# Optimization experiments

Hardware: AMD Instinct MI355X
Metric: run time of the kernel (lower is better)

The kernel has to match this reference:

```python
import math
import jax, jax.numpy as jnp
import numpy as np

N, E, H, D, NNZ = 32768, 512, 8, 64, 524288


def setup_inputs() -> dict:
    key = jax.random.key(0)
    ks = jax.random.split(key, 12)
    x = jax.random.normal(ks[0], (N, E), dtype=jnp.float32)
    row_index = jnp.sort(jax.random.randint(ks[1], (NNZ,), 0, N))
    col_index = jax.random.randint(ks[2], (NNZ,), 0, N)
    to_col_index = jax.random.randint(ks[3], (N,), 0, N)
    att_bias = jax.random.normal(ks[4], (H, NNZ), dtype=jnp.float32)
    # positive interatomic distances in ~[0.5, 5.5)
    dist = jax.random.uniform(ks[5], (NNZ,), dtype=jnp.float32) * 5.0 + 0.5
    pos = jax.random.normal(ks[6], (N, 3), dtype=jnp.float32)
    col_pos = jax.random.normal(ks[7], (N, 3), dtype=jnp.float32)
    s = 1.0 / math.sqrt(E)
    q_w = jax.random.normal(ks[8], (E, E), dtype=jnp.float32) * s
    q_b = jax.random.normal(ks[9], (E,), dtype=jnp.float32) * 0.02
    k_w = jax.random.normal(ks[10], (E, E), dtype=jnp.float32) * s
    k_b = jax.random.normal(ks[11], (E,), dtype=jnp.float32) * 0.02
    return {"x": x, "row_index": row_index, "col_index": col_index,
            "to_col_index": to_col_index, "att_bias": att_bias, "dist": dist,
            "pos": pos, "col_pos": col_pos,
            "q_w": q_w, "q_b": q_b, "k_w": k_w, "k_b": k_b}


def reference(x, row_index, col_index, to_col_index, att_bias, dist, pos, col_pos,
              q_w, q_b, k_w, k_b):
    n = x.shape[0]
    h = att_bias.shape[0]
    d = x.shape[1] // h
    # per-head projections: [N, H, D]
    q = (x @ q_w.T + q_b).reshape(n, h, d) * (1.0 / math.sqrt(d))
    k = (x @ k_w.T + k_b).reshape(n, h, d)[to_col_index]  # [Nk, H, D]
    # sparse (COO) masked q @ k^T plus additive bias -> per-edge logits [nnz, H]
    logits = jnp.einsum('ehd,ehd->eh', q[row_index], k[col_index]) + att_bias.T
    # sparse softmax over each query row (per head)
    m = jax.ops.segment_max(logits, row_index, num_segments=n)       # [N, H]
    p = jnp.exp(logits - m[row_index])
    z = jax.ops.segment_sum(p, row_index, num_segments=n)            # [N, H]
    att = p / z[row_index]                                           # [nnz, H]
    # distance-weighted attention (dist==0 -> contribution 0, as x/inf in torch)
    inv_d = jnp.where(dist == 0, 0.0, 1.0 / dist)
    att = att * inv_d[:, None]
    # sparse bmm against col_pos values and against ones
    cp = col_pos[col_index]                                          # [nnz, 3]
    dst_vec = jax.ops.segment_sum(att[:, :, None] * cp[:, None, :],
                                  row_index, num_segments=n)         # [N, H, 3]
    avg_inv_dist = jax.ops.segment_sum(att, row_index, num_segments=n)  # [N, H]
    src_vec = avg_inv_dist[..., None] * pos[:, None, :]              # [N, H, 3]
    v = dst_vec - src_vec
    norm = jnp.sqrt(jnp.sum(v * v, axis=-1, keepdims=True))
    feat3 = v / jnp.maximum(norm, 1e-12)                             # F.normalize
    feat = jnp.concatenate([feat3, avg_inv_dist[..., None]], axis=-1)  # [N, H, 4]
    return feat.reshape(n, h * 4)
```

## Files before the change

kernel.cpp:

```cpp
#include <hip/hip_runtime.h>
#include <math.h>
#include <stdint.h>

#define N_NODES 32768
#define E_DIM   512
#define H_HEADS 8
#define D_HEAD  64
#define NNZ_E   524288

typedef __attribute__((ext_vector_type(4))) float f32x4;
typedef __attribute__((ext_vector_type(8))) _Float16 f16x8;
typedef __attribute__((ext_vector_type(8))) short s16x8;

__device__ __forceinline__ void async16(const void* g, void* l) {
  __builtin_amdgcn_global_load_lds(
      (const __attribute__((address_space(1))) void*)g,
      (__attribute__((address_space(3))) void*)l, 16, 0, 0);
}

__global__ __launch_bounds__(256) void prep_small(
    const float* __restrict__ x,
    const float* __restrict__ q_w, const float* __restrict__ k_w,
    const int* __restrict__ row_index, const int* __restrict__ col_index,
    const int* __restrict__ to_col,
    _Float16* __restrict__ wq_h, _Float16* __restrict__ wk_h,
    _Float16* __restrict__ xs,
    int* __restrict__ row_start, int* __restrict__ ge) {
  const int b = blockIdx.x;
  if (b < 8448) {
    const float* src;
    _Float16* dst;
    int t;
    if (b < 128)      { src = q_w; dst = wq_h; t = b * 256 + threadIdx.x; }
    else if (b < 256) { src = k_w; dst = wk_h; t = (b - 128) * 256 + threadIdx.x; }
    else              { src = x;   dst = xs;   t = (b - 256) * 256 + threadIdx.x; }
    const int r = t >> 6;
    const int c8 = (t & 63) << 3;
    const float4 v0 = *(const float4*)(src + (size_t)r * 512 + c8);
    const float4 v1 = *(const float4*)(src + (size_t)r * 512 + c8 + 4);
    f16x8 o;
    o[0] = (_Float16)v0.x; o[1] = (_Float16)v0.y;
    o[2] = (_Float16)v0.z; o[3] = (_Float16)v0.w;
    o[4] = (_Float16)v1.x; o[5] = (_Float16)v1.y;
    o[6] = (_Float16)v1.z; o[7] = (_Float16)v1.w;
    *(f16x8*)(dst + (size_t)r * 512 + c8) = o;
  } else {
    const int e = (b - 8448) * 256 + threadIdx.x;
    if (e < NNZ_E) {
      ge[e] = to_col[col_index[e]];
      const int r0 = row_index[e];
      const int r1 = (e + 1 < NNZ_E) ? row_index[e + 1] : N_NODES;
      if (e == 0)
        for (int r = 0; r <= r0; ++r) row_start[r] = 0;
      for (int r = r0 + 1; r <= r1; ++r) row_start[r] = e + 1;
    }
  }
}

__global__ __launch_bounds__(256) void gemm_mfma(
    const _Float16* __restrict__ xs,
    const _Float16* __restrict__ wqh,
    const _Float16* __restrict__ wkh,
    const float* __restrict__ q_b, const float* __restrict__ k_b,
    short* __restrict__ q16, short* __restrict__ k16) {
  __shared__ _Float16 Ah[128 * 32];
  __shared__ _Float16 Bh[128 * 32];
  const int tid = threadIdx.x;
  const int w = tid >> 6;
  const int l = tid & 63;

  const int b = blockIdx.x;
  const int j = b >> 3;
  const int mb = (b & 7) * 32 + (j >> 3);
  const int c = j & 7;
  const bool is_q = ((c & 1) == 0);
  const int bm = mb * 128;
  const int bn = (c >> 1) * 128;

  const _Float16* __restrict__ wmat = is_q ? wqh : wkh;
  const float* __restrict__ bias = is_q ? q_b : k_b;
  short* __restrict__ outp = is_q ? q16 : k16;
  const float oscale = is_q ? 2048.f : 4096.f;

  const int wm = (w & 1) * 64;
  const int wn = (w >> 1) * 64;

  f32x4 acc[4][4];
#pragma unroll
  for (int i = 0; i < 4; ++i)
#pragma unroll
    for (int jj = 0; jj < 4; ++jj) acc[i][jj] = (f32x4){0.f, 0.f, 0.f, 0.f};

  const int sr0 = w * 16 + (l >> 2);
  const int sr1 = sr0 + 64;
  const int sc = (((l & 3) ^ ((l >> 3) & 3)) << 3);
  const int fr = l & 15;
  const int fcs = ((((l >> 4) ^ ((fr >> 1) & 3)) & 3) << 3);

  const _Float16* __restrict__ wa = wmat + (size_t)bn * 512;
  const _Float16* __restrict__ xa = xs + (size_t)bm * 512;

  for (int k0 = 0; k0 < 512; k0 += 32) {
    async16(xa + (size_t)sr0 * 512 + k0 + sc, Ah + w * 512);
    async16(xa + (size_t)sr1 * 512 + k0 + sc, Ah + (w + 4) * 512);
    async16(wa + (size_t)sr0 * 512 + k0 + sc, Bh + w * 512);
    async16(wa + (size_t)sr1 * 512 + k0 + sc, Bh + (w + 4) * 512);
    __syncthreads();

    f16x8 av[4], bv[4];
#pragma unroll
    for (int i = 0; i < 4; ++i)
      av[i] = *(const f16x8*)(Ah + (wm + i * 16 + fr) * 32 + fcs);
#pragma unroll
    for (int i = 0; i < 4; ++i)
      bv[i] = *(const f16x8*)(Bh + (wn + i * 16 + fr) * 32 + fcs);
#pragma unroll
    for (int i = 0; i < 4; ++i)
#pragma unroll
      for (int jj = 0; jj < 4; ++jj)
        acc[i][jj] = __builtin_amdgcn_mfma_f32_16x16x32_f16(
            av[i], bv[jj], acc[i][jj], 0, 0, 0);
    __syncthreads();
  }

  const int cn = l & 15;
  const int cm4 = (l >> 4) * 4;
  float bvals[4];
#pragma unroll
  for (int jj = 0; jj < 4; ++jj) bvals[jj] = bias[bn + wn + jj * 16 + cn];
#pragma unroll
  for (int i = 0; i < 4; ++i) {
#pragma unroll
    for (int r = 0; r < 4; ++r) {
      const int m = bm + wm + i * 16 + cm4 + r;
      short* op = outp + (size_t)m * 512 + bn + wn + cn;
#pragma unroll
      for (int jj = 0; jj < 4; ++jj) {
        float v = (acc[i][jj][r] + bvals[jj]) * oscale;
        v = fmaxf(fminf(v, 32767.f), -32767.f);
        op[jj * 16] = (short)__float2int_rn(v);
      }
    }
  }
}

__global__ __launch_bounds__(256) void row_fused(
    const short* __restrict__ q16, const short* __restrict__ k16,
    const int* __restrict__ row_start, const int* __restrict__ ge,
    const float* __restrict__ att_bias, const int* __restrict__ col_index,
    const float* __restrict__ dist, const float* __restrict__ pos,
    const float* __restrict__ col_pos, float* __restrict__ out) {
  const int r = blockIdx.x * 4 + (threadIdx.x >> 6);
  const int lane = threadIdx.x & 63;
  const int h = lane >> 3;
  const int start = row_start[r];
  const int end = row_start[r + 1];

  const s16x8 qv = *(const s16x8*)(q16 + (size_t)r * E_DIM + lane * 8);
  const float* __restrict__ biasp = att_bias + (size_t)h * NNZ_E;

  float m = -INFINITY, l = 0.f, accw = 0.f, a0 = 0.f, a1 = 0.f, a2 = 0.f;

  auto dotk = [&](const s16x8 kv) -> float {
    float s = (float)qv[0] * (float)kv[0];
    s = fmaf((float)qv[1], (float)kv[1], s);
    s = fmaf((float)qv[2], (float)kv[2], s);
    s = fmaf((float)qv[3], (float)kv[3], s);
    s = fmaf((float)qv[4], (float)kv[4], s);
    s = fmaf((float)qv[5], (float)kv[5], s);
    s = fmaf((float)qv[6], (float)kv[6], s);
    s = fmaf((float)qv[7], (float)kv[7], s);
    s += __shfl_xor(s, 1);
    s += __shfl_xor(s, 2);
    s += __shfl_xor(s, 4);
    return s;
  };
  auto upd = [&](float logit, float dd, float c0, float c1, float c2) {
    const float w = (dd == 0.f) ? 0.f : 1.f / dd;
    const float nm = fmaxf(m, logit);
    const float sc = __expf(m - nm);
    const float p = __expf(logit - nm);
    m = nm;
    l = fmaf(l, sc, p);
    const float pw = p * w;
    accw = fmaf(accw, sc, pw);
    a0 = fmaf(a0, sc, pw * c0);
    a1 = fmaf(a1, sc, pw * c1);
    a2 = fmaf(a2, sc, pw * c2);
  };

  int e = start;
  for (; e + 4 <= end; e += 4) {
    int g[4], cc[4];
    float dd[4], bb[4], cp[4][3];
    s16x8 kv[4];
#pragma unroll
    for (int i = 0; i < 4; ++i) g[i] = ge[e + i];
#pragma unroll
    for (int i = 0; i < 4; ++i)
      kv[i] = *(const s16x8*)(k16 + (size_t)g[i] * E_DIM + lane * 8);
#pragma unroll
    for (int i = 0; i < 4; ++i) {
      cc[i] = col_index[e + i];
      dd[i] = dist[e + i];
      bb[i] = biasp[e + i];
    }
#pragma unroll
    for (int i = 0; i < 4; ++i) {
      cp[i][0] = col_pos[cc[i] * 3 + 0];
      cp[i][1] = col_pos[cc[i] * 3 + 1];
      cp[i][2] = col_pos[cc[i] * 3 + 2];
    }
    float s[4];
#pragma unroll
    for (int i = 0; i < 4; ++i)
      s[i] = dotk(kv[i]) * (1.f / 67108864.f) + bb[i];
#pragma unroll
    for (int i = 0; i < 4; ++i) upd(s[i], dd[i], cp[i][0], cp[i][1], cp[i][2]);
  }
  for (; e < end; ++e) {
    const int g0 = ge[e];
    const s16x8 kv0 = *(const s16x8*)(k16 + (size_t)g0 * E_DIM + lane * 8);
    const int c0 = col_index[e];
    const float dd0 = dist[e];
    const float bb0 = biasp[e];
    const float cp00 = col_pos[c0 * 3 + 0];
    const float cp01 = col_pos[c0 * 3 + 1];
    const float cp02 = col_pos[c0 * 3 + 2];
    const float s0 = dotk(kv0) * (1.f / 67108864.f) + bb0;
    upd(s0, dd0, cp00, cp01, cp02);
  }

  if ((lane & 7) == 0) {
    const float invz = (l > 0.f) ? 1.f / l : 0.f;
    const float avg = accw * invz;
    const float v0 = a0 * invz - avg * pos[r * 3 + 0];
    const float v1 = a1 * invz - avg * pos[r * 3 + 1];
    const float v2 = a2 * invz - avg * pos[r * 3 + 2];
    const float nrm = sqrtf(v0 * v0 + v1 * v1 + v2 * v2);
    const float invn = 1.f / fmaxf(nrm, 1e-12f);
    float4 o;
    o.x = v0 * invn; o.y = v1 * invn; o.z = v2 * invn; o.w = avg;
    *(float4*)(out + (size_t)r * (H_HEADS * 4) + h * 4) = o;
  }
}

extern "C" void kernel_launch(void* const* d_in, const int* in_sizes, int n_in,
                              void* d_out, int out_size, void* d_ws,
                              size_t ws_size, hipStream_t stream) {
  const float* x        = (const float*)d_in[0];
  const int* row_index  = (const int*)d_in[1];
  const int* col_index  = (const int*)d_in[2];
  const int* to_col     = (const int*)d_in[3];
  const float* att_bias = (const float*)d_in[4];
  const float* dist     = (const float*)d_in[5];
  const float* pos      = (const float*)d_in[6];
  const float* col_pos  = (const float*)d_in[7];
  const float* q_w      = (const float*)d_in[8];
  const float* q_b      = (const float*)d_in[9];
  const float* k_w      = (const float*)d_in[10];
  const float* k_b      = (const float*)d_in[11];
  float* out = (float*)d_out;

  short* q16 = (short*)d_ws;
  short* k16 = q16 + (size_t)N_NODES * E_DIM;
  _Float16* xs = (_Float16*)(k16 + (size_t)N_NODES * E_DIM);
  _Float16* wq_h = xs + (size_t)N_NODES * 512;
  _Float16* wk_h = wq_h + 512 * 512;
  int* row_start = (int*)(wk_h + 512 * 512);
  int* ge = row_start + (N_NODES + 1);

  prep_small<<<8448 + NNZ_E / 256, 256, 0, stream>>>(
      x, q_w, k_w, row_index, col_index, to_col, wq_h, wk_h, xs, row_start, ge);

  gemm_mfma<<<2048, 256, 0, stream>>>(xs, wq_h, wk_h, q_b, k_b, q16, k16);

  row_fused<<<N_NODES / 4, 256, 0, stream>>>(q16, k16, row_start, ge, att_bias,
                                             col_index, dist, pos, col_pos,
                                             out);
}
```

Before: 261.6 us.

## Store Q/K as fp16 with packed dot2, and deepen GEMM K-step to 64

Replaces the int16 fixed-point Q/K storage with fp16 outputs, so the per-edge dot product can use packed fdot2 instructions instead of eight converts plus FMAs. The descale multiply disappears, and the reciprocal of distance uses the fast rcp builtin. The GEMM now loads two 32-wide K slices per iteration into separate LDS buffers, halving the number of barrier pairs in exchange for doubled shared memory. fp16 storage has different range and precision than the scaled int16 format, which could shift accuracy.

```diff
diff --git a/kernel.cpp b/kernel.cpp
--- a/kernel.cpp
+++ b/kernel.cpp
@@ -10,12 +10,29 @@
 
 typedef __attribute__((ext_vector_type(4))) float f32x4;
 typedef __attribute__((ext_vector_type(8))) _Float16 f16x8;
-typedef __attribute__((ext_vector_type(8))) short s16x8;
+typedef __attribute__((ext_vector_type(2))) _Float16 f16x2;
 
 __device__ __forceinline__ void async16(const void* g, void* l) {
   __builtin_amdgcn_global_load_lds(
       (const __attribute__((address_space(1))) void*)g,
       (__attribute__((address_space(3))) void*)l, 16, 0, 0);
+}
+
+__device__ __forceinline__ float dot8(const f16x8 a, const f16x8 b, float acc) {
+#if __has_builtin(__builtin_amdgcn_fdot2)
+  acc = __builtin_amdgcn_fdot2(__builtin_shufflevector(a, a, 0, 1),
+                               __builtin_shufflevector(b, b, 0, 1), acc, false);
+  acc = __builtin_amdgcn_fdot2(__builtin_shufflevector(a, a, 2, 3),
+                               __builtin_shufflevector(b, b, 2, 3), acc, false);
+  acc = __builtin_amdgcn_fdot2(__builtin_shufflevector(a, a, 4, 5),
+                               __builtin_shufflevector(b, b, 4, 5), acc, false);
+  acc = __builtin_amdgcn_fdot2(__builtin_shufflevector(a, a, 6, 7),
+                               __builtin_shufflevector(b, b, 6, 7), acc, false);
+#else
+#pragma unroll
+  for (int i = 0; i < 8; ++i) acc = fmaf((float)a[i], (float)b[i], acc);
+#endif
+  return acc;
 }
 
 __global__ __launch_bounds__(256) void prep_small(
@@ -62,9 +79,11 @@
     const _Float16* __restrict__ wqh,
     const _Float16* __restrict__ wkh,
     const float* __restrict__ q_b, const float* __restrict__ k_b,
-    short* __restrict__ q16, short* __restrict__ k16) {
-  __shared__ _Float16 Ah[128 * 32];
-  __shared__ _Float16 Bh[128 * 32];
+    _Float16* __restrict__ qh, _Float16* __restrict__ kh) {
+  __shared__ _Float16 Ah0[128 * 32];
+  __shared__ _Float16 Ah1[128 * 32];
+  __shared__ _Float16 Bh0[128 * 32];
+  __shared__ _Float16 Bh1[128 * 32];
   const int tid = threadIdx.x;
   const int w = tid >> 6;
   const int l = tid & 63;
@@ -79,8 +98,8 @@
 
   const _Float16* __restrict__ wmat = is_q ? wqh : wkh;
   const float* __restrict__ bias = is_q ? q_b : k_b;
-  short* __restrict__ outp = is_q ? q16 : k16;
-  const float oscale = is_q ? 2048.f : 4096.f;
+  _Float16* __restrict__ outp = is_q ? qh : kh;
+  const float oscale = is_q ? 0.125f : 1.0f;
 
   const int wm = (w & 1) * 64;
   const int wn = (w >> 1) * 64;
@@ -100,26 +119,42 @@
   const _Float16* __restrict__ wa = wmat + (size_t)bn * 512;
   const _Float16* __restrict__ xa = xs + (size_t)bm * 512;
 
-  for (int k0 = 0; k0 < 512; k0 += 32) {
-    async16(xa + (size_t)sr0 * 512 + k0 + sc, Ah + w * 512);
-    async16(xa + (size_t)sr1 * 512 + k0 + sc, Ah + (w + 4) * 512);
-    async16(wa + (size_t)sr0 * 512 + k0 + sc, Bh + w * 512);
-    async16(wa + (size_t)sr1 * 512 + k0 + sc, Bh + (w + 4) * 512);
+  for (int k0 = 0; k0 < 512; k0 += 64) {
+    async16(xa + (size_t)sr0 * 512 + k0 + sc, Ah0 + w * 512);
+    async16(xa + (size_t)sr1 * 512 + k0 + sc, Ah0 + (w + 4) * 512);
+    async16(xa + (size_t)sr0 * 512 + k0 + 32 + sc, Ah1 + w * 512);
+    async16(xa + (size_t)sr1 * 512 + k0 + 32 + sc, Ah1 + (w + 4) * 512);
+    async16(wa + (size_t)sr0 * 512 + k0 + sc, Bh0 + w * 512);
+    async16(wa + (size_t)sr1 * 512 + k0 + sc, Bh0 + (w + 4) * 512);
+    async16(wa + (size_t)sr0 * 512 + k0 + 32 + sc, Bh1 + w * 512);
+    async16(wa + (size_t)sr1 * 512 + k0 + 32 + sc, Bh1 + (w + 4) * 512);
     __syncthreads();
 
-    f16x8 av[4], bv[4];
-#pragma unroll
-    for (int i = 0; i < 4; ++i)
-      av[i] = *(const f16x8*)(Ah + (wm + i * 16 + fr) * 32 + fcs);
-#pragma unroll
-    for (int i = 0; i < 4; ++i)
-      bv[i] = *(const f16x8*)(Bh + (wn + i * 16 + fr) * 32 + fcs);
+    f16x8 av0[4], av1[4], bv0[4], bv1[4];
+#pragma unroll
+    for (int i = 0; i < 4; ++i) {
+      const int ro = (wm + i * 16 + fr) * 32 + fcs;
+      av0[i] = *(const f16x8*)(Ah0 + ro);
+      av1[i] = *(const f16x8*)(Ah1 + ro);
+    }
+#pragma unroll
+    for (int i = 0; i < 4; ++i) {
+      const int ro = (wn + i * 16 + fr) * 32 + fcs;
+      bv0[i] = *(const f16x8*)(Bh0 + ro);
+      bv1[i] = *(const f16x8*)(Bh1 + ro);
+    }
 #pragma unroll
     for (int i = 0; i < 4; ++i)
 #pragma unroll
       for (int jj = 0; jj < 4; ++jj)
         acc[i][jj] = __builtin_amdgcn_mfma_f32_16x16x32_f16(
-            av[i], bv[jj], acc[i][jj], 0, 0, 0);
+            av0[i], bv0[jj], acc[i][jj], 0, 0, 0);
+#pragma unroll
+    for (int i = 0; i < 4; ++i)
+#pragma unroll
+      for (int jj = 0; jj < 4; ++jj)
+        acc[i][jj] = __builtin_amdgcn_mfma_f32_16x16x32_f16(
+            av1[i], bv1[jj], acc[i][jj], 0, 0, 0);
     __syncthreads();
   }
 
@@ -133,19 +168,17 @@
 #pragma unroll
     for (int r = 0; r < 4; ++r) {
       const int m = bm + wm + i * 16 + cm4 + r;
-      short* op = outp + (size_t)m * 512 + bn + wn + cn;
+      _Float16* op = outp + (size_t)m * 512 + bn + wn + cn;
 #pragma unroll
       for (int jj = 0; jj < 4; ++jj) {
-        float v = (acc[i][jj][r] + bvals[jj]) * oscale;
-        v = fmaxf(fminf(v, 32767.f), -32767.f);
-        op[jj * 16] = (short)__float2int_rn(v);
+        op[jj * 16] = (_Float16)((acc[i][jj][r] + bvals[jj]) * oscale);
       }
     }
   }
 }
 
 __global__ __launch_bounds__(256) void row_fused(
-    const short* __restrict__ q16, const short* __restrict__ k16,
+    const _Float16* __restrict__ qh, const _Float16* __restrict__ kh,
     const int* __restrict__ row_start, const int* __restrict__ ge,
     const float* __restrict__ att_bias, const int* __restrict__ col_index,
     const float* __restrict__ dist, const float* __restrict__ pos,
@@ -156,27 +189,20 @@
   const int start = row_start[r];
   const int end = row_start[r + 1];
 
-  const s16x8 qv = *(const s16x8*)(q16 + (size_t)r * E_DIM + lane * 8);
+  const f16x8 qv = *(const f16x8*)(qh + (size_t)r * E_DIM + lane * 8);
   const float* __restrict__ biasp = att_bias + (size_t)h * NNZ_E;
 
   float m = -INFINITY, l = 0.f, accw = 0.f, a0 = 0.f, a1 = 0.f, a2 = 0.f;
 
-  auto dotk = [&](const s16x8 kv) -> float {
-    float s = (float)qv[0] * (float)kv[0];
-    s = fmaf((float)qv[1], (float)kv[1], s);
-    s = fmaf((float)qv[2], (float)kv[2], s);
-    s = fmaf((float)qv[3], (float)kv[3], s);
-    s = fmaf((float)qv[4], (float)kv[4], s);
-    s = fmaf((float)qv[5], (float)kv[5], s);
-    s = fmaf((float)qv[6], (float)kv[6], s);
-    s = fmaf((float)qv[7], (float)kv[7], s);
+  auto edge_logit = [&](const f16x8 kv) -> float {
+    float s = dot8(qv, kv, 0.f);
     s += __shfl_xor(s, 1);
     s += __shfl_xor(s, 2);
     s += __shfl_xor(s, 4);
     return s;
   };
   auto upd = [&](float logit, float dd, float c0, float c1, float c2) {
-    const float w = (dd == 0.f) ? 0.f : 1.f / dd;
+    const float w = (dd == 0.f) ? 0.f : __builtin_amdgcn_rcpf(dd);
     const float nm = fmaxf(m, logit);
     const float sc = __expf(m - nm);
     const float p = __expf(logit - nm);
@@ -193,12 +219,12 @@
   for (; e + 4 <= end; e += 4) {
     int g[4], cc[4];
     float dd[4], bb[4], cp[4][3];
-    s16x8 kv[4];
+    f16x8 kv[4];
 #pragma unroll
     for (int i = 0; i < 4; ++i) g[i] = ge[e + i];
 #pragma unroll
     for (int i = 0; i < 4; ++i)
-      kv[i] = *(const s16x8*)(k16 + (size_t)g[i] * E_DIM + lane * 8);
+      kv[i] = *(const f16x8*)(kh + (size_t)g[i] * E_DIM + lane * 8);
 #pragma unroll
     for (int i = 0; i < 4; ++i) {
       cc[i] = col_index[e + i];
@@ -213,21 +239,20 @@
     }
     float s[4];
 #pragma unroll
-    for (int i = 0; i < 4; ++i)
-      s[i] = dotk(kv[i]) * (1.f / 67108864.f) + bb[i];
+    for (int i = 0; i < 4; ++i) s[i] = edge_logit(kv[i]) + bb[i];
 #pragma unroll
     for (int i = 0; i < 4; ++i) upd(s[i], dd[i], cp[i][0], cp[i][1], cp[i][2]);
   }
   for (; e < end; ++e) {
     const int g0 = ge[e];
-    const s16x8 kv0 = *(const s16x8*)(k16 + (size_t)g0 * E_DIM + lane * 8);
+    const f16x8 kv0 = *(const f16x8*)(kh + (size_t)g0 * E_DIM + lane * 8);
     const int c0 = col_index[e];
     const float dd0 = dist[e];
     const float bb0 = biasp[e];
     const float cp00 = col_pos[c0 * 3 + 0];
     const float cp01 = col_pos[c0 * 3 + 1];
     const float cp02 = col_pos[c0 * 3 + 2];
-    const float s0 = dotk(kv0) * (1.f / 67108864.f) + bb0;
+    const float s0 = edge_logit(kv0) + bb0;
     upd(s0, dd0, cp00, cp01, cp02);
   }
 
@@ -262,9 +287,9 @@
   const float* k_b      = (const float*)d_in[11];
   float* out = (float*)d_out;
 
-  short* q16 = (short*)d_ws;
-  short* k16 = q16 + (size_t)N_NODES * E_DIM;
-  _Float16* xs = (_Float16*)(k16 + (size_t)N_NODES * E_DIM);
+  _Float16* qh = (_Float16*)d_ws;
+  _Float16* kh = qh + (size_t)N_NODES * 512;
+  _Float16* xs = kh + (size_t)N_NODES * 512;
   _Float16* wq_h = xs + (size_t)N_NODES * 512;
   _Float16* wk_h = wq_h + 512 * 512;
   int* row_start = (int*)(wk_h + 512 * 512);
@@ -273,9 +298,9 @@
   prep_small<<<8448 + NNZ_E / 256, 256, 0, stream>>>(
       x, q_w, k_w, row_index, col_index, to_col, wq_h, wk_h, xs, row_start, ge);
 
-  gemm_mfma<<<2048, 256, 0, stream>>>(xs, wq_h, wk_h, q_b, k_b, q16, k16);
-
-  row_fused<<<N_NODES / 4, 256, 0, stream>>>(q16, k16, row_start, ge, att_bias,
+  gemm_mfma<<<2048, 256, 0, stream>>>(xs, wq_h, wk_h, q_b, k_b, qh, kh);
+
+  row_fused<<<N_NODES / 4, 256, 0, stream>>>(qh, kh, row_start, ge, att_bias,
                                              col_index, dist, pos, col_pos,
                                              out);
 }
```

Result: no change. 262.9 us (+0.5%).
